# Kernel optimization log

Measured on AMD Instinct MI355X. Metric: run time of the kernel, lower is better.

The kernel has to match this reference:

```python
import jax, jax.numpy as jnp
import numpy as np

NLVL = 8
C = 64          # channel_siz
FIN = 16        # in_filter_siz  = in_siz  / 2**nlvl
FOUT = 16       # out_filter_siz = out_siz / 2**nlvl
B = 512
IN_SIZ = 4096
STD = 0.1  # keeps 8 relu-matmul levels numerically stable (0.1*sqrt(2C)~1.1 gain/level)


def setup_inputs() -> dict:
    key = jax.random.key(0)
    k0, k1, k2, k3, k4, k5 = jax.random.split(key, 6)
    n_lvl_filters = 2 ** (NLVL + 1) - 2  # 510: level lvl occupies [2^lvl-2 : 2^(lvl+1)-2]
    return {
        "in_data": jax.random.normal(k0, (B, IN_SIZ), dtype=jnp.float32),
        "W_in": jax.random.normal(k1, (FIN, C), dtype=jnp.float32) * STD,
        "b_in": jax.random.normal(k2, (C,), dtype=jnp.float32) * STD,
        "W_lvl": jax.random.normal(k3, (n_lvl_filters, 2, C, C), dtype=jnp.float32) * STD,
        "b_lvl": jax.random.normal(k4, (n_lvl_filters, C), dtype=jnp.float32) * STD,
        "Fea": jax.random.normal(k5, (2 ** NLVL, C, FOUT), dtype=jnp.float32) * STD,
    }


def reference(in_data, W_in, b_in, W_lvl, b_lvl, Fea):
    b = in_data.shape[0]
    # Input interpolation: conv1d(filter (FIN,1,C), stride FIN) on (b, 2^nlvl*FIN, 1)
    # == per-block matmul on (b, 2^nlvl, FIN).
    x = in_data.reshape(b, 2 ** NLVL, FIN)
    V = jax.nn.relu(jnp.einsum("bkf,fc->bkc", x, W_in) + b_in)  # (b, 2^nlvl, C)
    # State V: (b, K, T, C) where K = 2^lvl boxes, T = 2^(nlvl-lvl) positions.
    V = V[:, None]  # lvl 0: (b, 1, 2^nlvl, C)
    for lvl in range(1, NLVL + 1):
        K = 2 ** lvl
        off = K - 2
        W = W_lvl[off:off + K]          # (K, 2, C, C)
        bb = b_lvl[off:off + K]         # (K, C)
        T = V.shape[2] // 2
        pairs = V.reshape(b, K // 2, T, 2, C)      # stride-2 conv pairs
        pairs = jnp.repeat(pairs, 2, axis=1)       # both children share the parent
        V = jax.nn.relu(jnp.einsum("bktsc,kscd->bktd", pairs, W) + bb[:, None, :])
    # Output dense per box: (b, 2^nlvl, C) x (2^nlvl, C, FOUT)
    out = jnp.einsum("bkc,kcf->bkf", V[:, :, 0, :], Fea)
    return out.reshape(b, 2 ** NLVL * FOUT, 1)
```

## Files before the change

### kernel.cpp

```cpp
#include <hip/hip_runtime.h>

typedef __attribute__((ext_vector_type(8))) short short8;
typedef __attribute__((ext_vector_type(4))) float f32x4;

#define NLVL 8

__device__ __forceinline__ unsigned short f2bf(float f) {
    union { float f; unsigned u; } v; v.f = f;
    unsigned r = v.u + 0x7FFFu + ((v.u >> 16) & 1u);
    return (unsigned short)(r >> 16);
}
__device__ __forceinline__ float bf2f(unsigned short h) {
    union { unsigned u; float f; } v; v.u = ((unsigned)h) << 16;
    return v.f;
}

__global__ __launch_bounds__(256) void k_convw(const float* __restrict__ W_lvl,
                                               unsigned short* __restrict__ Wt) {
    __shared__ float buf[128 * 65];
    const int kf = blockIdx.x;
    const int i  = threadIdx.x;
    const float* src = W_lvl + (size_t)kf * 8192;
    for (int m = 0; m < 32; ++m) {
        int idx = m * 256 + i;
        int kin = idx >> 6, d = idx & 63;
        buf[kin * 65 + d] = src[idx];
    }
    __syncthreads();
    unsigned short* dst = Wt + (size_t)kf * 16384;
    for (int m = 0; m < 64; ++m) {
        int o = m * 256 + i;
        int d = o >> 8;
        int kin2 = o & 255;
        int kin = kin2 & 127;
        float val = buf[kin * 65 + d];
        unsigned short hi = f2bf(val);
        unsigned short outv = (kin2 >> 7) ? f2bf(val - bf2f(hi)) : hi;
        dst[o] = outv;
    }
}

__global__ __launch_bounds__(256) void k_lvl0(const float* __restrict__ x,
                                              const float* __restrict__ W_in,
                                              const float* __restrict__ b_in,
                                              unsigned short* __restrict__ V0) {
    __shared__ float wl[16 * 64];
    __shared__ float bl[64];
    __shared__ float xl[16 * 16];
    const int i = threadIdx.x;
    for (int m = 0; m < 4; ++m) wl[m * 256 + i] = W_in[m * 256 + i];
    if (i < 64) bl[i] = b_in[i];
    const int row0 = blockIdx.x * 16;
    xl[i] = x[(size_t)row0 * 16 + i];
    __syncthreads();
    const int r  = i >> 4;
    const int c0 = (i & 15) * 4;
    float a0 = bl[c0], a1 = bl[c0 + 1], a2 = bl[c0 + 2], a3 = bl[c0 + 3];
#pragma unroll
    for (int f = 0; f < 16; ++f) {
        float xv = xl[r * 16 + f];
        const float* wrow = &wl[f * 64 + c0];
        a0 += xv * wrow[0]; a1 += xv * wrow[1]; a2 += xv * wrow[2]; a3 += xv * wrow[3];
    }
    size_t ob = (size_t)(row0 + r) * 64 + c0;
    V0[ob]     = f2bf(fmaxf(a0, 0.f));
    V0[ob + 1] = f2bf(fmaxf(a1, 0.f));
    V0[ob + 2] = f2bf(fmaxf(a2, 0.f));
    V0[ob + 3] = f2bf(fmaxf(a3, 0.f));
}

__global__ __launch_bounds__(256, 3) void k_level(const unsigned short* __restrict__ Vprev,
                                                  unsigned short* __restrict__ Vnext,
                                                  const unsigned short* __restrict__ Wt,
                                                  const float* __restrict__ b_lvl,
                                                  int lvl) {
    const int T   = 1 << (8 - lvl);
    const int lgT = 8 - lvl;
    const int off = (1 << lvl) - 2;
    const int p   = blockIdx.y;
    const int tid = threadIdx.x;
    const int w   = tid >> 6;
    const int l   = tid & 63;
    const int q   = l >> 4;
    const int ln  = l & 15;

    short8 bw[2][8];
    {
        const unsigned short* wbase =
            Wt + (size_t)(off + 2 * p) * 16384 + (size_t)(w * 16 + ln) * 256 + q * 8;
#pragma unroll
        for (int s = 0; s < 2; ++s)
#pragma unroll
            for (int kk = 0; kk < 8; ++kk)
                bw[s][kk] = *(const short8*)(wbase + s * 16384 + kk * 32);
    }
    const float bias0 = b_lvl[(off + 2 * p) * 64 + w * 16 + ln];
    const float bias1 = b_lvl[(off + 2 * p + 1) * 64 + w * 16 + ln];

#pragma unroll 2
    for (int m = 0; m < 4; ++m) {
        const int r = blockIdx.x * 64 + m * 16 + ln;
        const int b = r >> lgT;
        const int t = r & (T - 1);
        const unsigned short* Abase =
            Vprev + ((size_t)b << 14) + ((size_t)p << (lgT + 7)) + (size_t)t * 128 + q * 8;
        short8 a[4];
#pragma unroll
        for (int kk = 0; kk < 4; ++kk)
            a[kk] = *(const short8*)(Abase + kk * 32);

        f32x4 acc0 = {0.f, 0.f, 0.f, 0.f};
        f32x4 acc1 = {0.f, 0.f, 0.f, 0.f};
#pragma unroll
        for (int kk = 0; kk < 8; ++kk)
            acc0 = __builtin_amdgcn_mfma_f32_16x16x32_bf16(a[kk & 3], bw[0][kk], acc0, 0, 0, 0);
#pragma unroll
        for (int kk = 0; kk < 8; ++kk)
            acc1 = __builtin_amdgcn_mfma_f32_16x16x32_bf16(a[kk & 3], bw[1][kk], acc1, 0, 0, 0);

#pragma unroll
        for (int j = 0; j < 4; ++j) {
            const int rg = blockIdx.x * 64 + m * 16 + q * 4 + j;
            const int bb = rg >> lgT;
            const int tt = rg & (T - 1);
            const size_t base = ((size_t)bb << 14) + (size_t)(2 * p) * ((size_t)T << 6) +
                                (size_t)tt * 64 + w * 16 + ln;
            Vnext[base] = f2bf(fmaxf(acc0[j] + bias0, 0.f));
            Vnext[base + ((size_t)T << 6)] = f2bf(fmaxf(acc1[j] + bias1, 0.f));
        }
    }
}

__global__ __launch_bounds__(256) void k_final(const unsigned short* __restrict__ V8,
                                               const float* __restrict__ Fea,
                                               float* __restrict__ out) {
    __shared__ float fl[64 * 16];
    __shared__ unsigned short vl[16 * 64];
    const int k  = blockIdx.x;
    const int b0 = blockIdx.y * 16;
    const int i  = threadIdx.x;
    for (int m = 0; m < 4; ++m) fl[m * 256 + i] = Fea[(size_t)k * 1024 + m * 256 + i];
    {
        int idx = i * 4;
        int bl2 = idx >> 6, c = idx & 63;
        const unsigned short* src = V8 + ((size_t)(b0 + bl2) << 14) + k * 64 + c;
        *(uint2*)&vl[idx] = *(const uint2*)src;
    }
    __syncthreads();
    const int bl2 = i >> 4, f = i & 15;
    float acc = 0.f;
#pragma unroll
    for (int c = 0; c < 64; ++c)
        acc += bf2f(vl[bl2 * 64 + c]) * fl[c * 16 + f];
    out[(size_t)(b0 + bl2) * 4096 + (size_t)k * 16 + f] = acc;
}

extern "C" void kernel_launch(void* const* d_in, const int* in_sizes, int n_in,
                              void* d_out, int out_size, void* d_ws, size_t ws_size,
                              hipStream_t stream) {
    const float* in_data = (const float*)d_in[0];
    const float* W_in    = (const float*)d_in[1];
    const float* b_in    = (const float*)d_in[2];
    const float* W_lvl   = (const float*)d_in[3];
    const float* b_lvl   = (const float*)d_in[4];
    const float* Fea     = (const float*)d_in[5];
    float* out = (float*)d_out;

    unsigned short* Wt = (unsigned short*)d_ws;
    unsigned short* Va = (unsigned short*)((char*)d_ws + 16711680);
    unsigned short* Vb = (unsigned short*)((char*)d_ws + 16711680 + 16777216);

    k_convw<<<510, 256, 0, stream>>>(W_lvl, Wt);
    k_lvl0<<<8192, 256, 0, stream>>>(in_data, W_in, b_in, Va);

    const unsigned short* cur = Va;
    unsigned short* nxt = Vb;
    for (int lvl = 1; lvl <= NLVL; ++lvl) {
        int T = 1 << (8 - lvl);
        dim3 grid(8 * T, 1 << (lvl - 1));
        k_level<<<grid, 256, 0, stream>>>(cur, nxt, Wt, b_lvl, lvl);
        unsigned short* tmp = (unsigned short*)cur;
        cur = nxt;
        nxt = tmp;
    }
    k_final<<<dim3(256, 32), 256, 0, stream>>>(cur, Fea, out);
}
```

Measured before the change: 257.6 us.

## Fuse all stages into one persistent cooperative kernel with grid syncs

Replaces the eleven separate launches (weight conversion, level 0, eight tree levels, final dense) with a single cooperative persistent kernel that loops over work tiles and separates stages with grid.sync. Level tiles now stage the activation rows through swizzled LDS before the MFMA loop, and weights are reloaded per output child inside the tile loop. This targets launch gaps and tail effects across small kernels. In exchange it adds grid-wide barrier cost, limits the grid to resident blocks, and loses some per-level occupancy tuning.

```diff
diff --git a/kernel.cpp b/kernel.cpp
--- a/kernel.cpp
+++ b/kernel.cpp
@@ -1,9 +1,12 @@
 #include <hip/hip_runtime.h>
+#include <hip/hip_cooperative_groups.h>
+
+namespace cg = cooperative_groups;
 
 typedef __attribute__((ext_vector_type(8))) short short8;
 typedef __attribute__((ext_vector_type(4))) float f32x4;
 
-#define NLVL 8
+#define LDS_BYTES 33280
 
 __device__ __forceinline__ unsigned short f2bf(float f) {
     union { float f; unsigned u; } v; v.f = f;
@@ -15,144 +18,153 @@
     return v.f;
 }
 
-__global__ __launch_bounds__(256) void k_convw(const float* __restrict__ W_lvl,
-                                               unsigned short* __restrict__ Wt) {
-    __shared__ float buf[128 * 65];
-    const int kf = blockIdx.x;
-    const int i  = threadIdx.x;
-    const float* src = W_lvl + (size_t)kf * 8192;
-    for (int m = 0; m < 32; ++m) {
-        int idx = m * 256 + i;
-        int kin = idx >> 6, d = idx & 63;
-        buf[kin * 65 + d] = src[idx];
+__global__ __launch_bounds__(256, 4) void k_fused(
+    const float* __restrict__ in_data, const float* __restrict__ W_in,
+    const float* __restrict__ b_in, const float* __restrict__ W_lvl,
+    const float* __restrict__ b_lvl, const float* __restrict__ Fea,
+    float* __restrict__ out, unsigned short* __restrict__ Wt,
+    unsigned short* __restrict__ Va, unsigned short* __restrict__ Vb)
+{
+    extern __shared__ char lds[];
+    const int tid = threadIdx.x;
+    cg::grid_group grid = cg::this_grid();
+
+    {
+        float* buf = (float*)lds;
+        for (int kf = blockIdx.x; kf < 510; kf += gridDim.x) {
+            __syncthreads();
+            const float* src = W_lvl + (size_t)kf * 8192;
+            for (int m = 0; m < 32; ++m) {
+                int idx = m * 256 + tid;
+                int kin = idx >> 6, d = idx & 63;
+                buf[kin * 65 + d] = src[idx];
+            }
+            __syncthreads();
+            unsigned short* dst = Wt + (size_t)kf * 16384;
+            for (int m = 0; m < 64; ++m) {
+                int o = m * 256 + tid;
+                int d = o >> 8, kin2 = o & 255, kin = kin2 & 127;
+                float val = buf[kin * 65 + d];
+                unsigned short hi = f2bf(val);
+                dst[o] = (kin2 >> 7) ? f2bf(val - bf2f(hi)) : hi;
+            }
+        }
     }
     __syncthreads();
-    unsigned short* dst = Wt + (size_t)kf * 16384;
-    for (int m = 0; m < 64; ++m) {
-        int o = m * 256 + i;
-        int d = o >> 8;
-        int kin2 = o & 255;
-        int kin = kin2 & 127;
-        float val = buf[kin * 65 + d];
-        unsigned short hi = f2bf(val);
-        unsigned short outv = (kin2 >> 7) ? f2bf(val - bf2f(hi)) : hi;
-        dst[o] = outv;
-    }
-}
 
-__global__ __launch_bounds__(256) void k_lvl0(const float* __restrict__ x,
-                                              const float* __restrict__ W_in,
-                                              const float* __restrict__ b_in,
-                                              unsigned short* __restrict__ V0) {
-    __shared__ float wl[16 * 64];
-    __shared__ float bl[64];
-    __shared__ float xl[16 * 16];
-    const int i = threadIdx.x;
-    for (int m = 0; m < 4; ++m) wl[m * 256 + i] = W_in[m * 256 + i];
-    if (i < 64) bl[i] = b_in[i];
-    const int row0 = blockIdx.x * 16;
-    xl[i] = x[(size_t)row0 * 16 + i];
-    __syncthreads();
-    const int r  = i >> 4;
-    const int c0 = (i & 15) * 4;
-    float a0 = bl[c0], a1 = bl[c0 + 1], a2 = bl[c0 + 2], a3 = bl[c0 + 3];
+    {
+        float* wl = (float*)lds;
+        float* bl = wl + 1024;
+        float* xl = bl + 64;
+        for (int m = 0; m < 4; ++m) wl[m * 256 + tid] = W_in[m * 256 + tid];
+        if (tid < 64) bl[tid] = b_in[tid];
+        for (int rt = blockIdx.x; rt < 8192; rt += gridDim.x) {
+            const int row0 = rt * 16;
+            __syncthreads();
+            xl[tid] = in_data[(size_t)row0 * 16 + tid];
+            __syncthreads();
+            const int r = tid >> 4, c0 = (tid & 15) * 4;
+            float a0 = bl[c0], a1 = bl[c0+1], a2 = bl[c0+2], a3 = bl[c0+3];
 #pragma unroll
-    for (int f = 0; f < 16; ++f) {
-        float xv = xl[r * 16 + f];
-        const float* wrow = &wl[f * 64 + c0];
-        a0 += xv * wrow[0]; a1 += xv * wrow[1]; a2 += xv * wrow[2]; a3 += xv * wrow[3];
-    }
-    size_t ob = (size_t)(row0 + r) * 64 + c0;
-    V0[ob]     = f2bf(fmaxf(a0, 0.f));
-    V0[ob + 1] = f2bf(fmaxf(a1, 0.f));
-    V0[ob + 2] = f2bf(fmaxf(a2, 0.f));
-    V0[ob + 3] = f2bf(fmaxf(a3, 0.f));
-}
-
-__global__ __launch_bounds__(256, 3) void k_level(const unsigned short* __restrict__ Vprev,
-                                                  unsigned short* __restrict__ Vnext,
-                                                  const unsigned short* __restrict__ Wt,
-                                                  const float* __restrict__ b_lvl,
-                                                  int lvl) {
-    const int T   = 1 << (8 - lvl);
-    const int lgT = 8 - lvl;
-    const int off = (1 << lvl) - 2;
-    const int p   = blockIdx.y;
-    const int tid = threadIdx.x;
-    const int w   = tid >> 6;
-    const int l   = tid & 63;
-    const int q   = l >> 4;
-    const int ln  = l & 15;
-
-    short8 bw[2][8];
-    {
-        const unsigned short* wbase =
-            Wt + (size_t)(off + 2 * p) * 16384 + (size_t)(w * 16 + ln) * 256 + q * 8;
-#pragma unroll
-        for (int s = 0; s < 2; ++s)
-#pragma unroll
-            for (int kk = 0; kk < 8; ++kk)
-                bw[s][kk] = *(const short8*)(wbase + s * 16384 + kk * 32);
-    }
-    const float bias0 = b_lvl[(off + 2 * p) * 64 + w * 16 + ln];
-    const float bias1 = b_lvl[(off + 2 * p + 1) * 64 + w * 16 + ln];
-
-#pragma unroll 2
-    for (int m = 0; m < 4; ++m) {
-        const int r = blockIdx.x * 64 + m * 16 + ln;
-        const int b = r >> lgT;
-        const int t = r & (T - 1);
-        const unsigned short* Abase =
-            Vprev + ((size_t)b << 14) + ((size_t)p << (lgT + 7)) + (size_t)t * 128 + q * 8;
-        short8 a[4];
-#pragma unroll
-        for (int kk = 0; kk < 4; ++kk)
-            a[kk] = *(const short8*)(Abase + kk * 32);
-
-        f32x4 acc0 = {0.f, 0.f, 0.f, 0.f};
-        f32x4 acc1 = {0.f, 0.f, 0.f, 0.f};
-#pragma unroll
-        for (int kk = 0; kk < 8; ++kk)
-            acc0 = __builtin_amdgcn_mfma_f32_16x16x32_bf16(a[kk & 3], bw[0][kk], acc0, 0, 0, 0);
-#pragma unroll
-        for (int kk = 0; kk < 8; ++kk)
-            acc1 = __builtin_amdgcn_mfma_f32_16x16x32_bf16(a[kk & 3], bw[1][kk], acc1, 0, 0, 0);
-
-#pragma unroll
-        for (int j = 0; j < 4; ++j) {
-            const int rg = blockIdx.x * 64 + m * 16 + q * 4 + j;
-            const int bb = rg >> lgT;
-            const int tt = rg & (T - 1);
-            const size_t base = ((size_t)bb << 14) + (size_t)(2 * p) * ((size_t)T << 6) +
-                                (size_t)tt * 64 + w * 16 + ln;
-            Vnext[base] = f2bf(fmaxf(acc0[j] + bias0, 0.f));
-            Vnext[base + ((size_t)T << 6)] = f2bf(fmaxf(acc1[j] + bias1, 0.f));
+            for (int f = 0; f < 16; ++f) {
+                float xv = xl[r * 16 + f];
+                const float* wr = &wl[f * 64 + c0];
+                a0 += xv*wr[0]; a1 += xv*wr[1]; a2 += xv*wr[2]; a3 += xv*wr[3];
+            }
+            size_t ob = (size_t)(row0 + r) * 64 + c0;
+            Va[ob]   = f2bf(fmaxf(a0, 0.f));
+            Va[ob+1] = f2bf(fmaxf(a1, 0.f));
+            Va[ob+2] = f2bf(fmaxf(a2, 0.f));
+            Va[ob+3] = f2bf(fmaxf(a3, 0.f));
         }
     }
-}
+    grid.sync();
 
-__global__ __launch_bounds__(256) void k_final(const unsigned short* __restrict__ V8,
-                                               const float* __restrict__ Fea,
-                                               float* __restrict__ out) {
-    __shared__ float fl[64 * 16];
-    __shared__ unsigned short vl[16 * 64];
-    const int k  = blockIdx.x;
-    const int b0 = blockIdx.y * 16;
-    const int i  = threadIdx.x;
-    for (int m = 0; m < 4; ++m) fl[m * 256 + i] = Fea[(size_t)k * 1024 + m * 256 + i];
+    const int w  = tid >> 6;
+    const int l  = tid & 63;
+    const int q  = l >> 4;
+    const int ln = l & 15;
+    for (int lvl = 1; lvl <= 8; ++lvl) {
+        const int T = 1 << (8 - lvl), lgT = 8 - lvl, off = (1 << lvl) - 2;
+        const unsigned short* __restrict__ Vcur = (lvl & 1) ? Va : Vb;
+        unsigned short* __restrict__ Vnxt = (lvl & 1) ? Vb : Va;
+        for (int flat = blockIdx.x; flat < 1024; flat += gridDim.x) {
+            const int p = flat >> (11 - lvl);
+            const int x = flat & ((1 << (11 - lvl)) - 1);
+            __syncthreads();
+            for (int j = 0; j < 4; ++j) {
+                int c = tid + j * 256;
+                int row = c >> 4, sub = c & 15;
+                int rg = x * 64 + row;
+                int b = rg >> lgT, t = rg & (T - 1);
+                const unsigned short* g = Vcur + ((size_t)b << 14) +
+                    ((size_t)p << (lgT + 7)) + (size_t)t * 128 + sub * 8;
+                short8 v = *(const short8*)g;
+                *(short8*)(lds + row * 256 + ((sub * 16) ^ ((row & 7) << 4))) = v;
+            }
+            __syncthreads();
+#pragma unroll
+            for (int s = 0; s < 2; ++s) {
+                const int kf = off + 2 * p + s;
+                short8 bw[8];
+                const unsigned short* wbase =
+                    Wt + (size_t)kf * 16384 + (size_t)(w * 16 + ln) * 256 + q * 8;
+#pragma unroll
+                for (int kk = 0; kk < 8; ++kk)
+                    bw[kk] = *(const short8*)(wbase + kk * 32);
+                const float bias = b_lvl[kf * 64 + w * 16 + ln];
+#pragma unroll
+                for (int m = 0; m < 4; ++m) {
+                    short8 a[4];
+#pragma unroll
+                    for (int kk = 0; kk < 4; ++kk) {
+                        int row = m * 16 + ln;
+                        a[kk] = *(const short8*)(lds + row * 256 +
+                                 ((q * 16 + kk * 64) ^ ((row & 7) << 4)));
+                    }
+                    f32x4 acc = {0.f, 0.f, 0.f, 0.f};
+#pragma unroll
+                    for (int kk = 0; kk < 8; ++kk)
+                        acc = __builtin_amdgcn_mfma_f32_16x16x32_bf16(
+                            a[kk & 3], bw[kk], acc, 0, 0, 0);
+#pragma unroll
+                    for (int j = 0; j < 4; ++j) {
+                        int rg = x * 64 + m * 16 + q * 4 + j;
+                        int bb = rg >> lgT, tt = rg & (T - 1);
+                        Vnxt[((size_t)bb << 14) +
+                             (size_t)(2 * p + s) * ((size_t)T << 6) +
+                             (size_t)tt * 64 + w * 16 + ln] =
+                            f2bf(fmaxf(acc[j] + bias, 0.f));
+                    }
+                }
+            }
+        }
+        grid.sync();
+    }
+
     {
-        int idx = i * 4;
-        int bl2 = idx >> 6, c = idx & 63;
-        const unsigned short* src = V8 + ((size_t)(b0 + bl2) << 14) + k * 64 + c;
-        *(uint2*)&vl[idx] = *(const uint2*)src;
+        float* fl = (float*)lds;
+        unsigned short* vl = (unsigned short*)(lds + 4096);
+        for (int it = blockIdx.x; it < 8192; it += gridDim.x) {
+            const int k = it & 255, b0 = (it >> 8) * 16;
+            __syncthreads();
+            for (int m = 0; m < 4; ++m)
+                fl[m * 256 + tid] = Fea[(size_t)k * 1024 + m * 256 + tid];
+            {
+                int idx = tid * 4;
+                int bl2 = idx >> 6, c = idx & 63;
+                const unsigned short* src = Va + ((size_t)(b0 + bl2) << 14) + k * 64 + c;
+                *(uint2*)&vl[idx] = *(const uint2*)src;
+            }
+            __syncthreads();
+            const int bl2 = tid >> 4, f = tid & 15;
+            float acc = 0.f;
+#pragma unroll
+            for (int c = 0; c < 64; ++c)
+                acc += bf2f(vl[bl2 * 64 + c]) * fl[c * 16 + f];
+            out[(size_t)(b0 + bl2) * 4096 + (size_t)k * 16 + f] = acc;
+        }
     }
-    __syncthreads();
-    const int bl2 = i >> 4, f = i & 15;
-    float acc = 0.f;
-#pragma unroll
-    for (int c = 0; c < 64; ++c)
-        acc += bf2f(vl[bl2 * 64 + c]) * fl[c * 16 + f];
-    out[(size_t)(b0 + bl2) * 4096 + (size_t)k * 16 + f] = acc;
 }
 
 extern "C" void kernel_launch(void* const* d_in, const int* in_sizes, int n_in,
@@ -170,18 +182,16 @@
     unsigned short* Va = (unsigned short*)((char*)d_ws + 16711680);
     unsigned short* Vb = (unsigned short*)((char*)d_ws + 16711680 + 16777216);
 
-    k_convw<<<510, 256, 0, stream>>>(W_lvl, Wt);
-    k_lvl0<<<8192, 256, 0, stream>>>(in_data, W_in, b_in, Va);
+    int maxPerCU = 0;
+    hipOccupancyMaxActiveBlocksPerMultiprocessor(&maxPerCU, k_fused, 256,
+                                                 (size_t)LDS_BYTES);
+    if (maxPerCU < 1) maxPerCU = 1;
+    int nb = maxPerCU * 256;
+    if (nb > 1024) nb = 1024;
 
-    const unsigned short* cur = Va;
-    unsigned short* nxt = Vb;
-    for (int lvl = 1; lvl <= NLVL; ++lvl) {
-        int T = 1 << (8 - lvl);
-        dim3 grid(8 * T, 1 << (lvl - 1));
-        k_level<<<grid, 256, 0, stream>>>(cur, nxt, Wt, b_lvl, lvl);
-        unsigned short* tmp = (unsigned short*)cur;
-        cur = nxt;
-        nxt = tmp;
-    }
-    k_final<<<dim3(256, 32), 256, 0, stream>>>(cur, Fea, out);
+    void* args[] = {(void*)&in_data, (void*)&W_in, (void*)&b_in, (void*)&W_lvl,
+                    (void*)&b_lvl, (void*)&Fea, (void*)&out, (void*)&Wt,
+                    (void*)&Va, (void*)&Vb};
+    hipLaunchCooperativeKernel(k_fused, dim3(nb), dim3(256), args,
+                               (unsigned int)LDS_BYTES, stream);
 }
```

Result: slower. 784.2 us (+204.4%).
